# Performance work log

Hardware: AMD Instinct MI355X
Metric: run time of the kernel (lower is better)

## Reference

```python
import jax, jax.numpy as jnp
import numpy as np

NUM_SINK = 8   # cfg.SINKHORN_ITERS
MASS = 0.9     # marginal value used for a and b


def _graph_conv(x, W_enc, b_enc, W1, b1, W2, b2, k):
    # Node encoder
    h = jax.nn.relu(x @ W_enc + b_enc)                       # [G,M,D]
    # kNN in embedding space (per graph)
    sq = jnp.sum(h * h, axis=-1)                             # [G,M]
    d2 = sq[:, :, None] + sq[:, None, :] - 2.0 * jnp.einsum('gmd,gnd->gmn', h, h)
    d2 = d2 + jnp.eye(h.shape[1], dtype=h.dtype) * 1e9       # exclude self-loop
    _, idx = jax.lax.top_k(-d2, k)                           # [G,M,k]
    neigh = jax.vmap(lambda hg, ig: hg[ig])(h, idx)          # [G,M,k,D]
    hc = jnp.broadcast_to(h[:, :, None, :], neigh.shape)
    e = jnp.concatenate([hc, neigh - hc], axis=-1)           # [G,M,k,2D]
    e = jax.nn.relu(e @ W1 + b1)                             # edge embed
    e = e @ W2 + b2                                          # back to D
    return jnp.max(e, axis=2)                                # max-aggregate over neighbors


def _sinkhorn(cost, lam):
    # log-domain unrolled Sinkhorn, batched over graphs; a=b=0.9 marginals
    log_p = -cost / lam                                      # [G,M,N]
    log_m = jnp.log(jnp.asarray(MASS, cost.dtype))
    for _ in range(NUM_SINK - 1):
        log_p = log_p - (jax.nn.logsumexp(log_p, axis=2, keepdims=True) - log_m)
        log_p = log_p - (jax.nn.logsumexp(log_p, axis=1, keepdims=True) - log_m)
    log_p = log_p - (jax.nn.logsumexp(log_p, axis=2, keepdims=True) - log_m)
    return jnp.exp(log_p)


def setup_inputs() -> dict:
    key = jax.random.key(0)
    ks = jax.random.split(key, 6)
    G, M, D = 64, 256, 256
    E = 256  # edge embed size
    inp = {
        'tra_x': jax.random.normal(ks[0], (G, M, D), jnp.float32),
        'det_x': jax.random.normal(ks[1], (G, M, D), jnp.float32),
        'W_enc': jax.random.normal(ks[2], (D, D), jnp.float32) / np.sqrt(D),
        'b_enc': jnp.zeros((D,), jnp.float32),
        'W1': jax.random.normal(ks[3], (2 * D, E), jnp.float32) / np.sqrt(2 * D),
        'b1': jnp.zeros((E,), jnp.float32),
        'W2': jax.random.normal(ks[4], (E, D), jnp.float32) / np.sqrt(E),
        'b2': jnp.zeros((D,), jnp.float32),
        'eplison': jnp.zeros((1,), jnp.float32),
        'k': 16,
    }
    return inp


def reference(tra_x, det_x, W_enc, b_enc, W1, b1, W2, b2, eplison, k):
    tra = _graph_conv(tra_x, W_enc, b_enc, W1, b1, W2, b2, k)  # [G,M,D]
    det = _graph_conv(det_x, W_enc, b_enc, W1, b1, W2, b2, k)  # [G,N,D]
    corr = jnp.einsum('gmd,gnd->gmn', tra, det)
    n1 = jnp.linalg.norm(tra, axis=-1)                         # [G,M]
    n2 = jnp.linalg.norm(det, axis=-1)                         # [G,N]
    cost = -corr / (n1[:, :, None] * n2[:, None, :])
    lam = jnp.exp(eplison[0]) + 0.03
    return _sinkhorn(cost, lam)                                # [G,M,N]
```

## Files before the change

kernel.cpp:

```cpp
#include <hip/hip_runtime.h>
#include <math.h>

#define NG 64
#define NM 256
#define ND 256
#define NK 16
#define NR (NG * NM)
#define NB 32

#define MASSF 0.9f

typedef __attribute__((ext_vector_type(8))) short bf16x8;
typedef __attribute__((ext_vector_type(4))) float f32x4;

static __device__ __forceinline__ short f2bf(float x) {
  union {
    float f;
    unsigned u;
  } v;
  v.f = x;
  unsigned r = v.u + 0x7FFFu + ((v.u >> 16) & 1u);
  return (short)(r >> 16);
}
static __device__ __forceinline__ float bf2f(short x) {
  union {
    unsigned u;
    float f;
  } v;
  v.u = ((unsigned)(unsigned short)x) << 16;
  return v.f;
}

__global__ __launch_bounds__(256) void prep_k(const float* __restrict__ W1,
                                              const float* __restrict__ b1,
                                              const float* __restrict__ W2,
                                              short* __restrict__ w2t, short* __restrict__ w1cat,
                                              float* __restrict__ biascat) {
  const int b = blockIdx.x, k = threadIdx.x;
  if (b < 256) {
    w2t[b * 256 + k] = f2bf(W2[(size_t)k * 256 + b]);
  } else {
    const int n = b - 256;
    float v;
    if (n < 256)
      v = W1[(size_t)k * 256 + n] - W1[(size_t)(k + 256) * 256 + n];
    else
      v = W1[(size_t)(k + 256) * 256 + (n - 256)];
    w1cat[(size_t)n * 256 + k] = f2bf(v);
    if (k == 0) biascat[n] = (n < 256) ? b1[n] : 0.f;
  }
}

__global__ __launch_bounds__(256) void gemm_nn2_k(const float* __restrict__ A,
                                                  const float* __restrict__ B,
                                                  const float* __restrict__ bias,
                                                  float* __restrict__ C,
                                                  short* __restrict__ Cbf) {
  __shared__ float As[2][16][68];
  __shared__ float Bs[2][16][128];
  const int tid = threadIdx.x;
  const int tx = tid & 15, ty = tid >> 4;
  const int m0 = blockIdx.y * 64, n0 = blockIdx.x * 128;
  const int arow = tid >> 2, akc = (tid & 3) * 4;
  const int bkr = tid >> 4, bcc = (tid & 15) * 4;
  float4 av, bv0, bv1;
  float acc[4][8] = {};
  auto gload = [&](int k0) {
    av = *(const float4*)&A[(size_t)(m0 + arow) * 256 + k0 + akc];
    bv0 = *(const float4*)&B[(size_t)(k0 + bkr) * 256 + n0 + bcc];
    bv1 = *(const float4*)&B[(size_t)(k0 + bkr) * 256 + n0 + 64 + bcc];
  };
  auto swrite = [&](int buf) {
    As[buf][akc + 0][arow] = av.x;
    As[buf][akc + 1][arow] = av.y;
    As[buf][akc + 2][arow] = av.z;
    As[buf][akc + 3][arow] = av.w;
    *(float4*)&Bs[buf][bkr][bcc] = bv0;
    *(float4*)&Bs[buf][bkr][64 + bcc] = bv1;
  };
  gload(0);
  swrite(0);
  __syncthreads();
  for (int s = 0; s < 16; ++s) {
    if (s < 15) gload((s + 1) * 16);
    const int buf = s & 1;
#pragma unroll
    for (int kk = 0; kk < 16; ++kk) {
      const float4 a0 = *(const float4*)&As[buf][kk][ty * 4];
      const float4 b0 = *(const float4*)&Bs[buf][kk][tx * 4];
      const float4 b1 = *(const float4*)&Bs[buf][kk][64 + tx * 4];
      const float aa[4] = {a0.x, a0.y, a0.z, a0.w};
      const float bb[8] = {b0.x, b0.y, b0.z, b0.w, b1.x, b1.y, b1.z, b1.w};
#pragma unroll
      for (int i = 0; i < 4; ++i)
#pragma unroll
        for (int j = 0; j < 8; ++j) acc[i][j] = fmaf(aa[i], bb[j], acc[i][j]);
    }
    if (s < 15) swrite((s + 1) & 1);
    __syncthreads();
  }
  const float4 bia0 = *(const float4*)&bias[n0 + tx * 4];
  const float4 bia1 = *(const float4*)&bias[n0 + 64 + tx * 4];
#pragma unroll
  for (int i = 0; i < 4; ++i) {
    const size_t row = (size_t)(m0 + ty * 4 + i);
    float4 o0 = {fmaxf(acc[i][0] + bia0.x, 0.f), fmaxf(acc[i][1] + bia0.y, 0.f),
                 fmaxf(acc[i][2] + bia0.z, 0.f), fmaxf(acc[i][3] + bia0.w, 0.f)};
    float4 o1 = {fmaxf(acc[i][4] + bia1.x, 0.f), fmaxf(acc[i][5] + bia1.y, 0.f),
                 fmaxf(acc[i][6] + bia1.z, 0.f), fmaxf(acc[i][7] + bia1.w, 0.f)};
    *(float4*)&C[row * 256 + n0 + tx * 4] = o0;
    *(float4*)&C[row * 256 + n0 + 64 + tx * 4] = o1;
    short4 h0 = {f2bf(o0.x), f2bf(o0.y), f2bf(o0.z), f2bf(o0.w)};
    short4 h1 = {f2bf(o1.x), f2bf(o1.y), f2bf(o1.z), f2bf(o1.w)};
    *(short4*)&Cbf[row * 256 + n0 + tx * 4] = h0;
    *(short4*)&Cbf[row * 256 + n0 + 64 + tx * 4] = h1;
  }
}

__global__ __launch_bounds__(256) void gemm_nt2_k(const float* __restrict__ h,
                                                  float* __restrict__ C) {
  const int bx = blockIdx.x, by = blockIdx.y, g = blockIdx.z;
  if (bx == 0 && by >= 2) return;
  __shared__ float As[2][16][68];
  __shared__ float Bs[2][16][128];
  const float* Ag = h + (size_t)g * NM * ND;
  float* Cg = C + (size_t)g * NM * NM;
  const int tid = threadIdx.x;
  const int tx = tid & 15, ty = tid >> 4;
  const int m0 = by * 64, n0 = bx * 128;
  const int arow = tid >> 2, akc = (tid & 3) * 4;
  const int brow = tid >> 1, bkc = (tid & 1) * 8;
  float4 av, bva, bvb;
  float acc[4][8] = {};
  auto gload = [&](int k0) {
    av = *(const float4*)&Ag[(size_t)(m0 + arow) * 256 + k0 + akc];
    bva = *(const float4*)&Ag[(size_t)(n0 + brow) * 256 + k0 + bkc];
    bvb = *(const float4*)&Ag[(size_t)(n0 + brow) * 256 + k0 + bkc + 4];
  };
  auto swrite = [&](int buf) {
    As[buf][akc + 0][arow] = av.x;
    As[buf][akc + 1][arow] = av.y;
    As[buf][akc + 2][arow] = av.z;
    As[buf][akc + 3][arow] = av.w;
    Bs[buf][bkc + 0][brow] = bva.x;
    Bs[buf][bkc + 1][brow] = bva.y;
    Bs[buf][bkc + 2][brow] = bva.z;
    Bs[buf][bkc + 3][brow] = bva.w;
    Bs[buf][bkc + 4][brow] = bvb.x;
    Bs[buf][bkc + 5][brow] = bvb.y;
    Bs[buf][bkc + 6][brow] = bvb.z;
    Bs[buf][bkc + 7][brow] = bvb.w;
  };
  gload(0);
  swrite(0);
  __syncthreads();
  for (int s = 0; s < 16; ++s) {
    if (s < 15) gload((s + 1) * 16);
    const int buf = s & 1;
#pragma unroll
    for (int kk = 0; kk < 16; ++kk) {
      const float4 a0 = *(const float4*)&As[buf][kk][ty * 4];
      const float4 b0 = *(const float4*)&Bs[buf][kk][tx * 4];
      const float4 b1 = *(const float4*)&Bs[buf][kk][64 + tx * 4];
      const float aa[4] = {a0.x, a0.y, a0.z, a0.w};
      const float bb[8] = {b0.x, b0.y, b0.z, b0.w, b1.x, b1.y, b1.z, b1.w};
#pragma unroll
      for (int i = 0; i < 4; ++i)
#pragma unroll
        for (int j = 0; j < 8; ++j) acc[i][j] = fmaf(aa[i], bb[j], acc[i][j]);
    }
    if (s < 15) swrite((s + 1) & 1);
    __syncthreads();
  }
#pragma unroll
  for (int i = 0; i < 4; ++i) {
    const size_t row = (size_t)(m0 + ty * 4 + i);
    float4 o0 = {acc[i][0], acc[i][1], acc[i][2], acc[i][3]};
    float4 o1 = {acc[i][4], acc[i][5], acc[i][6], acc[i][7]};
    *(float4*)&Cg[row * 256 + n0 + tx * 4] = o0;
    *(float4*)&Cg[row * 256 + n0 + 64 + tx * 4] = o1;
  }
  if (bx == 1 && by < 2) {
#pragma unroll
    for (int j = 0; j < 4; ++j) {
      const size_t col0 = (size_t)(n0 + tx * 4 + j);
      const size_t col1 = (size_t)(n0 + 64 + tx * 4 + j);
      float4 t0 = {acc[0][j], acc[1][j], acc[2][j], acc[3][j]};
      float4 t1 = {acc[0][4 + j], acc[1][4 + j], acc[2][4 + j], acc[3][4 + j]};
      *(float4*)&Cg[col0 * 256 + m0 + ty * 4] = t0;
      *(float4*)&Cg[col1 * 256 + m0 + ty * 4] = t1;
    }
  }
}

__global__ __launch_bounds__(256, 2) void mlp1_mfma_k(const short* __restrict__ A,
                                                      const short* __restrict__ Bt,
                                                      const float* __restrict__ biascat,
                                                      short* __restrict__ baseb,
                                                      short* __restrict__ n1b) {
  __shared__ char As[64 * 512];
  const int tid = threadIdx.x;
  const int l = tid & 63, wv = tid >> 6;
  const int r = l & 15, gq = l >> 4;
  const int m0 = blockIdx.y * 64, n0 = blockIdx.x * 128;
  bf16x8 bfr[2][8];
  float bv[2];
#pragma unroll
  for (int nt = 0; nt < 2; ++nt) {
    const int col = n0 + wv * 32 + nt * 16 + r;
    const short* wb = Bt + (size_t)col * 256 + gq * 8;
#pragma unroll
    for (int ks = 0; ks < 8; ++ks) bfr[nt][ks] = *(const bf16x8*)(wb + ks * 32);
    bv[nt] = biascat[col];
  }
  const int row = tid >> 2, ch = tid & 3;
  const char* ag = (const char*)(A + (size_t)(m0 + row) * 256) + ch * 128;
  char* lb = As + row * 512;
#pragma unroll
  for (int j = 0; j < 8; ++j)
    *(bf16x8*)(lb + (((ch * 128 + j * 16)) ^ ((row & 7) << 4))) = *(const bf16x8*)(ag + j * 16);
  __syncthreads();
  f32x4 acc[4][2];
#pragma unroll
  for (int mt = 0; mt < 4; ++mt)
#pragma unroll
    for (int nt = 0; nt < 2; ++nt) acc[mt][nt] = (f32x4){0.f, 0.f, 0.f, 0.f};
#pragma unroll
  for (int ks = 0; ks < 8; ++ks) {
    bf16x8 a[4];
#pragma unroll
    for (int mt = 0; mt < 4; ++mt)
      a[mt] = *(const bf16x8*)(As + (mt * 16 + r) * 512 + ((gq * 16 + ks * 64) ^ ((r & 7) << 4)));
#pragma unroll
    for (int mt = 0; mt < 4; ++mt)
#pragma unroll
      for (int nt = 0; nt < 2; ++nt)
        acc[mt][nt] = __builtin_amdgcn_mfma_f32_16x16x32_bf16(a[mt], bfr[nt][ks], acc[mt][nt], 0, 0, 0);
  }
  short* dst = (n0 < 256) ? baseb : n1b;
  const int cb = (n0 < 256) ? n0 : n0 - 256;
#pragma unroll
  for (int mt = 0; mt < 4; ++mt)
#pragma unroll
    for (int nt = 0; nt < 2; ++nt) {
      const int col = cb + wv * 32 + nt * 16 + r;
#pragma unroll
      for (int reg = 0; reg < 4; ++reg) {
        const int rw = m0 + mt * 16 + gq * 4 + reg;
        dst[(size_t)rw * 256 + col] = f2bf(acc[mt][nt][reg] + bv[nt]);
      }
    }
}

__global__ __launch_bounds__(256, 2) void cost_mfma_k(const short* __restrict__ featT,
                                                      const short* __restrict__ featD,
                                                      const float* __restrict__ nA,
                                                      const float* __restrict__ nB,
                                                      const float* __restrict__ eps,
                                                      float* __restrict__ P) {
  __shared__ char As[64 * 512];
  const int g = blockIdx.z;
  const short* A = featT + (size_t)g * NM * ND;
  const short* Bt = featD + (size_t)g * NM * ND;
  const int tid = threadIdx.x;
  const int l = tid & 63, wv = tid >> 6;
  const int r = l & 15, gq = l >> 4;
  const int m0 = blockIdx.y * 64, n0 = blockIdx.x * 128;
  bf16x8 bfr[2][8];
  float rnb[2];
#pragma unroll
  for (int nt = 0; nt < 2; ++nt) {
    const int col = n0 + wv * 32 + nt * 16 + r;
    const short* wb = Bt + (size_t)col * 256 + gq * 8;
#pragma unroll
    for (int ks = 0; ks < 8; ++ks) bfr[nt][ks] = *(const bf16x8*)(wb + ks * 32);
    rnb[nt] = 1.0f / nB[g * NM + col];
  }
  const int row = tid >> 2, ch = tid & 3;
  const char* ag = (const char*)(A + (size_t)(m0 + row) * 256) + ch * 128;
  char* lb = As + row * 512;
#pragma unroll
  for (int j = 0; j < 8; ++j)
    *(bf16x8*)(lb + (((ch * 128 + j * 16)) ^ ((row & 7) << 4))) = *(const bf16x8*)(ag + j * 16);
  __syncthreads();
  f32x4 acc[4][2];
#pragma unroll
  for (int mt = 0; mt < 4; ++mt)
#pragma unroll
    for (int nt = 0; nt < 2; ++nt) acc[mt][nt] = (f32x4){0.f, 0.f, 0.f, 0.f};
#pragma unroll
  for (int ks = 0; ks < 8; ++ks) {
    bf16x8 a[4];
#pragma unroll
    for (int mt = 0; mt < 4; ++mt)
      a[mt] = *(const bf16x8*)(As + (mt * 16 + r) * 512 + ((gq * 16 + ks * 64) ^ ((r & 7) << 4)));
#pragma unroll
    for (int mt = 0; mt < 4; ++mt)
#pragma unroll
      for (int nt = 0; nt < 2; ++nt)
        acc[mt][nt] = __builtin_amdgcn_mfma_f32_16x16x32_bf16(a[mt], bfr[nt][ks], acc[mt][nt], 0, 0, 0);
  }
  const float inv_lam = 1.0f / (expf(eps[0]) + 0.03f);
#pragma unroll
  for (int mt = 0; mt < 4; ++mt) {
    float ria[4];
#pragma unroll
    for (int reg = 0; reg < 4; ++reg)
      ria[reg] = inv_lam / nA[g * NM + m0 + mt * 16 + gq * 4 + reg];
#pragma unroll
    for (int nt = 0; nt < 2; ++nt) {
      const int col = n0 + wv * 32 + nt * 16 + r;
#pragma unroll
      for (int reg = 0; reg < 4; ++reg) {
        const int rw = m0 + mt * 16 + gq * 4 + reg;
        P[(size_t)g * NM * NM + (size_t)rw * 256 + col] =
            expf(acc[mt][nt][reg] * ria[reg] * rnb[nt]);
      }
    }
  }
}

__global__ __launch_bounds__(256) void rowsq_k(const float* __restrict__ h,
                                               float* __restrict__ sq) {
  const int w = threadIdx.x >> 6, lane = threadIdx.x & 63;
  const int row = blockIdx.x * 4 + w;
  float4 v = *(const float4*)&h[(size_t)row * ND + lane * 4];
  float s = v.x * v.x + v.y * v.y + v.z * v.z + v.w * v.w;
#pragma unroll
  for (int off = 32; off; off >>= 1) s += __shfl_xor(s, off);
  if (lane == 0) sq[row] = s;
}

__global__ __launch_bounds__(256) void normrow_bf_k(const short* __restrict__ feat,
                                                    float* __restrict__ nrm) {
  const int w = threadIdx.x >> 6, lane = threadIdx.x & 63;
  const int row = blockIdx.x * 4 + w;
  const short4 v = *(const short4*)&feat[(size_t)row * ND + lane * 4];
  const float a = bf2f(v.x), b = bf2f(v.y), c = bf2f(v.z), d = bf2f(v.w);
  float s = a * a + b * b + c * c + d * d;
#pragma unroll
  for (int off = 32; off; off >>= 1) s += __shfl_xor(s, off);
  if (lane == 0) nrm[row] = sqrtf(s);
}

__global__ __launch_bounds__(256) void topk_k(const float* __restrict__ S,
                                              const float* __restrict__ sq,
                                              int* __restrict__ idx) {
  const int w = threadIdx.x >> 6, lane = threadIdx.x & 63;
  const int row = blockIdx.x * 4 + w;
  const int g = row >> 8, m = row & 255;
  const float* Srow = S + (size_t)row * NM;
  const float* sqg = sq + g * NM;
  const float sm = sqg[m];
  const float4 sv = *(const float4*)&Srow[lane * 4];
  const float4 qv = *(const float4*)&sqg[lane * 4];
  float cand[4] = {sm + qv.x - 2.f * sv.x, sm + qv.y - 2.f * sv.y, sm + qv.z - 2.f * sv.z,
                   sm + qv.w - 2.f * sv.w};
#pragma unroll
  for (int t = 0; t < 4; ++t)
    if (lane * 4 + t == m) cand[t] = 1e30f;
  for (int rnd = 0; rnd < NK; ++rnd) {
    float bvv = cand[0];
    int bi = lane * 4;
#pragma unroll
    for (int t = 1; t < 4; ++t)
      if (cand[t] < bvv) {
        bvv = cand[t];
        bi = lane * 4 + t;
      }
#pragma unroll
    for (int off = 1; off < 64; off <<= 1) {
      const float ov = __shfl_xor(bvv, off);
      const int oi = __shfl_xor(bi, off);
      if (ov < bvv || (ov == bvv && oi < bi)) {
        bvv = ov;
        bi = oi;
      }
    }
    if (lane == 0) idx[(size_t)row * NK + rnd] = bi;
    if ((bi >> 2) == lane) cand[bi & 3] = 1e30f;
  }
}

__global__ __launch_bounds__(512, 4) void edgemlp_mfma4_k(
    const short* __restrict__ baseb, const short* __restrict__ n1b, const int* __restrict__ idx,
    const short* __restrict__ w2t, const float* __restrict__ b2, short* __restrict__ featbf) {
  __shared__ short E[2][32 * 256];
  __shared__ int sidx[NB * NK];
  const int tid = threadIdx.x;
  const int l = tid & 63, wv = tid >> 6;
  const int node0 = blockIdx.x * NB;
  const int g = node0 >> 8;
  const int r = l & 15, gq = l >> 4;
  sidx[tid] = idx[(size_t)node0 * NK + tid];
  bf16x8 bfr[2][8];
  float b2v[2];
#pragma unroll
  for (int t = 0; t < 2; ++t) {
    const int nb = wv * 2 + t;
    const short* wb = w2t + (size_t)(nb * 16 + r) * 256 + gq * 8;
#pragma unroll
    for (int ks = 0; ks < 8; ++ks) bfr[t][ks] = *(const bf16x8*)(wb + ks * 32);
    b2v[t] = b2[nb * 16 + r];
  }
  __syncthreads();
  const int j = tid >> 5;
  const int c = (tid & 31) * 8;
  const unsigned wboff = (unsigned)((c * 2) ^ ((j & 7) << 4));
  bf16x8 ns0, ns1;
  auto sload = [&](int s) {
    const int nb0 = s * 2;
    ns0 = *(const bf16x8*)(n1b + ((((size_t)g << 8) + sidx[nb0 * NK + j]) << 8) + c);
    ns1 = *(const bf16x8*)(n1b + ((((size_t)g << 8) + sidx[(nb0 + 1) * NK + j]) << 8) + c);
  };
  auto swrite = [&](int s) {
    char* eb = (char*)&E[s & 1][0];
    const int nb0 = s * 2;
    const bf16x8 b0 = *(const bf16x8*)(baseb + (((size_t)(node0 + nb0)) << 8) + c);
    const bf16x8 b1 = *(const bf16x8*)(baseb + (((size_t)(node0 + nb0 + 1)) << 8) + c);
    bf16x8 w0, w1;
#pragma unroll
    for (int q = 0; q < 8; ++q) {
      w0[q] = f2bf(fmaxf(bf2f(b0[q]) + bf2f(ns0[q]), 0.f));
      w1[q] = f2bf(fmaxf(bf2f(b1[q]) + bf2f(ns1[q]), 0.f));
    }
    *(bf16x8*)(eb + (size_t)j * 512 + wboff) = w0;
    *(bf16x8*)(eb + (size_t)(16 + j) * 512 + wboff) = w1;
  };
  sload(0);
  swrite(0);
  __syncthreads();
  for (int s = 0; s < NB / 2; ++s) {
    if (s + 1 < NB / 2) sload(s + 1);
    const char* eb = (const char*)&E[s & 1][0];
#pragma unroll
    for (int q = 0; q < 2; ++q) {
      f32x4 acc0 = (f32x4){0.f, 0.f, 0.f, 0.f};
      f32x4 acc1 = (f32x4){0.f, 0.f, 0.f, 0.f};
      const int rowb = (q * 16 + r) * 512;
#pragma unroll
      for (int ks = 0; ks < 8; ++ks) {
        const bf16x8 a = *(const bf16x8*)(eb + rowb + ((gq * 16 + ks * 64) ^ ((r & 7) << 4)));
        acc0 = __builtin_amdgcn_mfma_f32_16x16x32_bf16(a, bfr[0][ks], acc0, 0, 0, 0);
        acc1 = __builtin_amdgcn_mfma_f32_16x16x32_bf16(a, bfr[1][ks], acc1, 0, 0, 0);
      }
      const int nd = node0 + s * 2 + q;
      float m0v = fmaxf(fmaxf(acc0[0], acc0[1]), fmaxf(acc0[2], acc0[3]));
      m0v = fmaxf(m0v, __shfl_xor(m0v, 16));
      m0v = fmaxf(m0v, __shfl_xor(m0v, 32));
      float m1v = fmaxf(fmaxf(acc1[0], acc1[1]), fmaxf(acc1[2], acc1[3]));
      m1v = fmaxf(m1v, __shfl_xor(m1v, 16));
      m1v = fmaxf(m1v, __shfl_xor(m1v, 32));
      if (gq == 0) {
        featbf[((size_t)nd << 8) + (wv * 2 + 0) * 16 + r] = f2bf(m0v + b2v[0]);
        featbf[((size_t)nd << 8) + (wv * 2 + 1) * 16 + r] = f2bf(m1v + b2v[1]);
      }
    }
    if (s + 1 < NB / 2) swrite(s + 1);
    __syncthreads();
  }
}

__global__ __launch_bounds__(1024) void sinkhorn_k(float* __restrict__ P) {
  __shared__ float red[16][256];
  __shared__ float scal[256];
  const int t = threadIdx.x;
  const int tc = t & 15;
  const int trw = t >> 4;
  const int wv = t >> 6, l = t & 63;
  float* Pg = P + (size_t)blockIdx.x * NM * NM;
  float p[4][16];
#pragma unroll
  for (int i = 0; i < 4; ++i)
#pragma unroll
    for (int q = 0; q < 4; ++q)
      *(f32x4*)&p[i][q * 4] = *(const f32x4*)&Pg[(size_t)(trw * 4 + i) * NM + tc * 16 + q * 4];

  auto rowpass = [&]() {
#pragma unroll
    for (int i = 0; i < 4; ++i) {
      float s = p[i][0];
#pragma unroll
      for (int j = 1; j < 16; ++j) s += p[i][j];
      s += __shfl_xor(s, 1);
      s += __shfl_xor(s, 2);
      s += __shfl_xor(s, 4);
      s += __shfl_xor(s, 8);
      const float sc = MASSF / s;
#pragma unroll
      for (int j = 0; j < 16; ++j) p[i][j] *= sc;
    }
  };
  auto colpass = [&]() {
    float tmp[16];
#pragma unroll
    for (int j = 0; j < 16; ++j) tmp[j] = ((p[0][j] + p[1][j]) + (p[2][j] + p[3][j]));
#pragma unroll
    for (int j = 0; j < 16; ++j) {
      tmp[j] += __shfl_xor(tmp[j], 16);
      tmp[j] += __shfl_xor(tmp[j], 32);
    }
    if (l < 16) {
#pragma unroll
      for (int q = 0; q < 4; ++q)
        *(f32x4*)&red[wv][l * 16 + q * 4] = *(const f32x4*)&tmp[q * 4];
    }
    __syncthreads();
    if (t < 256) {
      float s = red[0][t];
#pragma unroll
      for (int w = 1; w < 16; ++w) s += red[w][t];
      scal[t] = MASSF / s;
    }
    __syncthreads();
#pragma unroll
    for (int j = 0; j < 16; ++j) {
      const float sc = scal[tc * 16 + j];
#pragma unroll
      for (int i = 0; i < 4; ++i) p[i][j] *= sc;
    }
    __syncthreads();
  };
  for (int it = 0; it < 7; ++it) {
    rowpass();
    colpass();
  }
  rowpass();
#pragma unroll
  for (int i = 0; i < 4; ++i)
#pragma unroll
    for (int q = 0; q < 4; ++q)
      *(f32x4*)&Pg[(size_t)(trw * 4 + i) * NM + tc * 16 + q * 4] = *(const f32x4*)&p[i][q * 4];
}

extern "C" void kernel_launch(void* const* d_in, const int* in_sizes, int n_in, void* d_out,
                              int out_size, void* d_ws, size_t ws_size, hipStream_t stream) {
  const float* tra_x = (const float*)d_in[0];
  const float* det_x = (const float*)d_in[1];
  const float* W_enc = (const float*)d_in[2];
  const float* b_enc = (const float*)d_in[3];
  const float* W1 = (const float*)d_in[4];
  const float* b1 = (const float*)d_in[5];
  const float* W2 = (const float*)d_in[6];
  const float* b2 = (const float*)d_in[7];
  const float* eps = (const float*)d_in[8];
  float* out = (float*)d_out;

  const size_t SZ = (size_t)NR * ND;
  float* h = (float*)d_ws;
  short* hbf = (short*)(h + SZ);
  short* baseb = hbf + SZ;
  short* n1b = baseb + SZ;
  short* featT = n1b + SZ;
  short* featD = featT + SZ;
  float* sq = (float*)(featD + SZ);
  float* nT = sq + NR;
  float* nD = nT + NR;
  int* idx = (int*)(nD + NR);
  short* w2t = (short*)(idx + (size_t)NR * NK);
  short* w1cat = w2t + 256 * 256;
  float* biascat = (float*)(w1cat + 512 * 256);
  float* S = out;

  const float* xs[2] = {tra_x, det_x};
  short* feats[2] = {featT, featD};
  float* nrms[2] = {nT, nD};

  prep_k<<<768, 256, 0, stream>>>(W1, b1, W2, w2t, w1cat, biascat);
  for (int s2 = 0; s2 < 2; ++s2) {
    gemm_nn2_k<<<dim3(2, 256), 256, 0, stream>>>(xs[s2], W_enc, b_enc, h, hbf);
    mlp1_mfma_k<<<dim3(4, 256), 256, 0, stream>>>(hbf, w1cat, biascat, baseb, n1b);
    rowsq_k<<<4096, 256, 0, stream>>>(h, sq);
    gemm_nt2_k<<<dim3(2, 4, NG), 256, 0, stream>>>(h, S);
    topk_k<<<4096, 256, 0, stream>>>(S, sq, idx);
    edgemlp_mfma4_k<<<NR / NB, 512, 0, stream>>>(baseb, n1b, idx, w2t, b2, feats[s2]);
    normrow_bf_k<<<4096, 256, 0, stream>>>(feats[s2], nrms[s2]);
  }
  cost_mfma_k<<<dim3(2, 4, NG), 256, 0, stream>>>(featT, featD, nT, nD, eps, out);
  sinkhorn_k<<<NG, 1024, 0, stream>>>(out);
}
```

Baseline: 398.7 us.

## Fuse feature norms into edge MLP, read sq from Gram diagonal, retile edge kernel

Result: slower. 568.4 us (+42.6%).

```diff
diff --git a/kernel.cpp b/kernel.cpp
--- a/kernel.cpp
+++ b/kernel.cpp
@@ -6,7 +6,7 @@
 #define ND 256
 #define NK 16
 #define NR (NG * NM)
-#define NB 32
+#define NB 16
 
 #define MASSF 0.9f
 
@@ -193,6 +193,12 @@
   }
 }
 
+__global__ __launch_bounds__(256) void diag_k(const float* __restrict__ S,
+                                              float* __restrict__ sq) {
+  const int g = blockIdx.x, m = threadIdx.x;
+  sq[g * 256 + m] = S[(size_t)g * NM * NM + (size_t)m * 257];
+}
+
 __global__ __launch_bounds__(256, 2) void mlp1_mfma_k(const short* __restrict__ A,
                                                       const short* __restrict__ Bt,
                                                       const float* __restrict__ biascat,
@@ -320,29 +326,6 @@
   }
 }
 
-__global__ __launch_bounds__(256) void rowsq_k(const float* __restrict__ h,
-                                               float* __restrict__ sq) {
-  const int w = threadIdx.x >> 6, lane = threadIdx.x & 63;
-  const int row = blockIdx.x * 4 + w;
-  float4 v = *(const float4*)&h[(size_t)row * ND + lane * 4];
-  float s = v.x * v.x + v.y * v.y + v.z * v.z + v.w * v.w;
-#pragma unroll
-  for (int off = 32; off; off >>= 1) s += __shfl_xor(s, off);
-  if (lane == 0) sq[row] = s;
-}
-
-__global__ __launch_bounds__(256) void normrow_bf_k(const short* __restrict__ feat,
-                                                    float* __restrict__ nrm) {
-  const int w = threadIdx.x >> 6, lane = threadIdx.x & 63;
-  const int row = blockIdx.x * 4 + w;
-  const short4 v = *(const short4*)&feat[(size_t)row * ND + lane * 4];
-  const float a = bf2f(v.x), b = bf2f(v.y), c = bf2f(v.z), d = bf2f(v.w);
-  float s = a * a + b * b + c * c + d * d;
-#pragma unroll
-  for (int off = 32; off; off >>= 1) s += __shfl_xor(s, off);
-  if (lane == 0) nrm[row] = sqrtf(s);
-}
-
 __global__ __launch_bounds__(256) void topk_k(const float* __restrict__ S,
                                               const float* __restrict__ sq,
                                               int* __restrict__ idx) {
@@ -382,82 +365,116 @@
   }
 }
 
-__global__ __launch_bounds__(512, 4) void edgemlp_mfma4_k(
+__global__ __launch_bounds__(256, 3) void edgemlp_mfma5_k(
     const short* __restrict__ baseb, const short* __restrict__ n1b, const int* __restrict__ idx,
-    const short* __restrict__ w2t, const float* __restrict__ b2, short* __restrict__ featbf) {
-  __shared__ short E[2][32 * 256];
+    const short* __restrict__ w2t, const float* __restrict__ b2, short* __restrict__ featbf,
+    float* __restrict__ nrm) {
+  __shared__ short E[2][2][512 * 8];
   __shared__ int sidx[NB * NK];
+  __shared__ float normp[NB][4];
   const int tid = threadIdx.x;
   const int l = tid & 63, wv = tid >> 6;
   const int node0 = blockIdx.x * NB;
   const int g = node0 >> 8;
   const int r = l & 15, gq = l >> 4;
   sidx[tid] = idx[(size_t)node0 * NK + tid];
-  bf16x8 bfr[2][8];
-  float b2v[2];
-#pragma unroll
-  for (int t = 0; t < 2; ++t) {
-    const int nb = wv * 2 + t;
+  bf16x8 bfr[4][8];
+  float b2v[4];
+#pragma unroll
+  for (int t = 0; t < 4; ++t) {
+    const int nb = wv * 4 + t;
     const short* wb = w2t + (size_t)(nb * 16 + r) * 256 + gq * 8;
 #pragma unroll
     for (int ks = 0; ks < 8; ++ks) bfr[t][ks] = *(const bf16x8*)(wb + ks * 32);
     b2v[t] = b2[nb * 16 + r];
   }
   __syncthreads();
-  const int j = tid >> 5;
-  const int c = (tid & 31) * 8;
-  const unsigned wboff = (unsigned)((c * 2) ^ ((j & 7) << 4));
-  bf16x8 ns0, ns1;
+  const int sr = tid & 15;
+  const int c1 = ((tid >> 4) & 3) * 8 + (tid >> 6) * 32;
+  bf16x8 nsa0, nsa1, nsb0, nsb1, ba0, ba1, bb0, bb1;
   auto sload = [&](int s) {
-    const int nb0 = s * 2;
-    ns0 = *(const bf16x8*)(n1b + ((((size_t)g << 8) + sidx[nb0 * NK + j]) << 8) + c);
-    ns1 = *(const bf16x8*)(n1b + ((((size_t)g << 8) + sidx[(nb0 + 1) * NK + j]) << 8) + c);
+    const int na = s * 2;
+    const short* pa = n1b + ((size_t)(g * NM + sidx[na * NK + sr])) * 256;
+    const short* pb = n1b + ((size_t)(g * NM + sidx[(na + 1) * NK + sr])) * 256;
+    nsa0 = *(const bf16x8*)(pa + c1);
+    nsa1 = *(const bf16x8*)(pa + c1 + 128);
+    nsb0 = *(const bf16x8*)(pb + c1);
+    nsb1 = *(const bf16x8*)(pb + c1 + 128);
+    const short* qa = baseb + (size_t)(node0 + na) * 256;
+    const short* qb = baseb + (size_t)(node0 + na + 1) * 256;
+    ba0 = *(const bf16x8*)(qa + c1);
+    ba1 = *(const bf16x8*)(qa + c1 + 128);
+    bb0 = *(const bf16x8*)(qb + c1);
+    bb1 = *(const bf16x8*)(qb + c1 + 128);
   };
   auto swrite = [&](int s) {
-    char* eb = (char*)&E[s & 1][0];
-    const int nb0 = s * 2;
-    const bf16x8 b0 = *(const bf16x8*)(baseb + (((size_t)(node0 + nb0)) << 8) + c);
-    const bf16x8 b1 = *(const bf16x8*)(baseb + (((size_t)(node0 + nb0 + 1)) << 8) + c);
-    bf16x8 w0, w1;
+    const int buf = s & 1;
+    bf16x8 w0, w1, w2, w3;
 #pragma unroll
     for (int q = 0; q < 8; ++q) {
-      w0[q] = f2bf(fmaxf(bf2f(b0[q]) + bf2f(ns0[q]), 0.f));
-      w1[q] = f2bf(fmaxf(bf2f(b1[q]) + bf2f(ns1[q]), 0.f));
-    }
-    *(bf16x8*)(eb + (size_t)j * 512 + wboff) = w0;
-    *(bf16x8*)(eb + (size_t)(16 + j) * 512 + wboff) = w1;
+      w0[q] = f2bf(fmaxf(bf2f(ba0[q]) + bf2f(nsa0[q]), 0.f));
+      w1[q] = f2bf(fmaxf(bf2f(ba1[q]) + bf2f(nsa1[q]), 0.f));
+      w2[q] = f2bf(fmaxf(bf2f(bb0[q]) + bf2f(nsb0[q]), 0.f));
+      w3[q] = f2bf(fmaxf(bf2f(bb1[q]) + bf2f(nsb1[q]), 0.f));
+    }
+    *(bf16x8*)&E[buf][0][tid * 8] = w0;
+    *(bf16x8*)&E[buf][0][(tid + 256) * 8] = w1;
+    *(bf16x8*)&E[buf][1][tid * 8] = w2;
+    *(bf16x8*)&E[buf][1][(tid + 256) * 8] = w3;
   };
   sload(0);
   swrite(0);
   __syncthreads();
   for (int s = 0; s < NB / 2; ++s) {
     if (s + 1 < NB / 2) sload(s + 1);
-    const char* eb = (const char*)&E[s & 1][0];
+    const int buf = s & 1;
+    const short* e0 = &E[buf][0][0];
+    const short* e1 = &E[buf][1][0];
+    f32x4 acc[2][4];
+#pragma unroll
+    for (int q = 0; q < 2; ++q)
+#pragma unroll
+      for (int t = 0; t < 4; ++t) acc[q][t] = (f32x4){0.f, 0.f, 0.f, 0.f};
+#pragma unroll
+    for (int ks = 0; ks < 8; ++ks) {
+      const bf16x8 a0 = *(const bf16x8*)(e0 + ks * 512 + l * 8);
+      const bf16x8 a1 = *(const bf16x8*)(e1 + ks * 512 + l * 8);
+#pragma unroll
+      for (int t = 0; t < 4; ++t) {
+        acc[0][t] = __builtin_amdgcn_mfma_f32_16x16x32_bf16(a0, bfr[t][ks], acc[0][t], 0, 0, 0);
+        acc[1][t] = __builtin_amdgcn_mfma_f32_16x16x32_bf16(a1, bfr[t][ks], acc[1][t], 0, 0, 0);
+      }
+    }
 #pragma unroll
     for (int q = 0; q < 2; ++q) {
-      f32x4 acc0 = (f32x4){0.f, 0.f, 0.f, 0.f};
-      f32x4 acc1 = (f32x4){0.f, 0.f, 0.f, 0.f};
-      const int rowb = (q * 16 + r) * 512;
-#pragma unroll
-      for (int ks = 0; ks < 8; ++ks) {
-        const bf16x8 a = *(const bf16x8*)(eb + rowb + ((gq * 16 + ks * 64) ^ ((r & 7) << 4)));
-        acc0 = __builtin_amdgcn_mfma_f32_16x16x32_bf16(a, bfr[0][ks], acc0, 0, 0, 0);
-        acc1 = __builtin_amdgcn_mfma_f32_16x16x32_bf16(a, bfr[1][ks], acc1, 0, 0, 0);
-      }
       const int nd = node0 + s * 2 + q;
-      float m0v = fmaxf(fmaxf(acc0[0], acc0[1]), fmaxf(acc0[2], acc0[3]));
-      m0v = fmaxf(m0v, __shfl_xor(m0v, 16));
-      m0v = fmaxf(m0v, __shfl_xor(m0v, 32));
-      float m1v = fmaxf(fmaxf(acc1[0], acc1[1]), fmaxf(acc1[2], acc1[3]));
-      m1v = fmaxf(m1v, __shfl_xor(m1v, 16));
-      m1v = fmaxf(m1v, __shfl_xor(m1v, 32));
+      float ss = 0.f;
+      short hv[4];
+#pragma unroll
+      for (int t = 0; t < 4; ++t) {
+        float m1 = fmaxf(fmaxf(acc[q][t][0], acc[q][t][1]), fmaxf(acc[q][t][2], acc[q][t][3]));
+        m1 = fmaxf(m1, __shfl_xor(m1, 16));
+        m1 = fmaxf(m1, __shfl_xor(m1, 32));
+        hv[t] = f2bf(m1 + b2v[t]);
+        const float o = bf2f(hv[t]);
+        ss += o * o;
+      }
       if (gq == 0) {
-        featbf[((size_t)nd << 8) + (wv * 2 + 0) * 16 + r] = f2bf(m0v + b2v[0]);
-        featbf[((size_t)nd << 8) + (wv * 2 + 1) * 16 + r] = f2bf(m1v + b2v[1]);
-      }
+#pragma unroll
+        for (int t = 0; t < 4; ++t) featbf[((size_t)nd << 8) + (wv * 4 + t) * 16 + r] = hv[t];
+      }
+      ss += __shfl_xor(ss, 1);
+      ss += __shfl_xor(ss, 2);
+      ss += __shfl_xor(ss, 4);
+      ss += __shfl_xor(ss, 8);
+      if (l == 0) normp[s * 2 + q][wv] = ss;
     }
     if (s + 1 < NB / 2) swrite(s + 1);
     __syncthreads();
+  }
+  if (tid < NB) {
+    float s = normp[tid][0] + normp[tid][1] + normp[tid][2] + normp[tid][3];
+    nrm[node0 + tid] = sqrtf(s);
   }
 }
 
@@ -570,11 +587,10 @@
   for (int s2 = 0; s2 < 2; ++s2) {
     gemm_nn2_k<<<dim3(2, 256), 256, 0, stream>>>(xs[s2], W_enc, b_enc, h, hbf);
     mlp1_mfma_k<<<dim3(4, 256), 256, 0, stream>>>(hbf, w1cat, biascat, baseb, n1b);
-    rowsq_k<<<4096, 256, 0, stream>>>(h, sq);
     gemm_nt2_k<<<dim3(2, 4, NG), 256, 0, stream>>>(h, S);
+    diag_k<<<NG, 256, 0, stream>>>(S, sq);
     topk_k<<<4096, 256, 0, stream>>>(S, sq, idx);
-    edgemlp_mfma4_k<<<NR / NB, 512, 0, stream>>>(baseb, n1b, idx, w2t, b2, feats[s2]);
-    normrow_bf_k<<<4096, 256, 0, stream>>>(feats[s2], nrms[s2]);
+    edgemlp_mfma5_k<<<NR / NB, 256, 0, stream>>>(baseb, n1b, idx, w2t, b2, feats[s2], nrms[s2]);
   }
   cost_mfma_k<<<dim3(2, 4, NG), 256, 0, stream>>>(featT, featD, nT, nD, eps, out);
   sinkhorn_k<<<NG, 1024, 0, stream>>>(out);
```
